# Kernel optimization log

Measured on AMD Instinct MI355X. Metric: run time of the kernel, lower is better.

Reference implementation:

```python
import jax, jax.numpy as jnp
import numpy as np

N = 20000


def _gcn_conv(x, edge_index, W, b):
    # add self loops
    n = x.shape[0]
    loops = jnp.arange(n, dtype=edge_index.dtype)
    row = jnp.concatenate([edge_index[0], loops])
    col = jnp.concatenate([edge_index[1], loops])
    # linear
    x = x @ W + b  # [N, C_out]
    # symmetric degree norm: deg computed over col (targets)
    deg = jax.ops.segment_sum(jnp.ones_like(col, dtype=x.dtype), col, num_segments=n)
    dinv = jnp.where(deg > 0, deg ** -0.5, 0.0)
    norm = dinv[row] * dinv[col]  # [E+N]
    # gather-scale-scatter (aggr='add' into col)
    msgs = norm[:, None] * x[row]  # [E+N, C_out]
    return jax.ops.segment_sum(msgs, col, num_segments=n)


def setup_inputs() -> dict:
    key = jax.random.key(0)
    k1, k2, k3, k4, k5, k6 = jax.random.split(key, 6)
    in_c, out_c = 256, 128
    hid = 2 * out_c
    x = jax.random.normal(k1, (N, in_c), dtype=jnp.float32)
    edge_index = jax.random.randint(k2, (2, 640000), 0, N, dtype=jnp.int64)
    s1 = 1.0 / np.sqrt(in_c)
    s2 = 1.0 / np.sqrt(hid)
    W1 = jax.random.uniform(k3, (in_c, hid), jnp.float32, -s1, s1)
    b1 = jax.random.uniform(k4, (hid,), jnp.float32, -s1, s1)
    W2 = jax.random.uniform(k5, (hid, out_c), jnp.float32, -s2, s2)
    b2 = jax.random.uniform(k6, (out_c,), jnp.float32, -s2, s2)
    return {"x": x, "edge_index": edge_index, "W1": W1, "b1": b1, "W2": W2, "b2": b2}


def reference(x, edge_index, W1, b1, W2, b2):
    h = jax.nn.relu(_gcn_conv(x, edge_index, W1, b1))
    return _gcn_conv(h, edge_index, W2, b2)
```

## Files before the change

### kernel.cpp

```cpp
#include <hip/hip_runtime.h>

#define CDIV(a,b) (((a)+(b)-1)/(b))

typedef _Float16 half4v __attribute__((ext_vector_type(4)));
typedef _Float16 half2v __attribute__((ext_vector_type(2)));
typedef _Float16 f16x8  __attribute__((ext_vector_type(8)));
typedef unsigned short ushort8v __attribute__((ext_vector_type(8)));
typedef float f32x4 __attribute__((ext_vector_type(4)));

__global__ void zero_kernel(int* __restrict__ p, int n) {
    int i = blockIdx.x * blockDim.x + threadIdx.x;
    if (i < n) p[i] = 0;
}

__global__ void hist_kernel(const int* __restrict__ coli, int* __restrict__ counts, int E) {
    int e = blockIdx.x * blockDim.x + threadIdx.x;
    if (e < E) atomicAdd(&counts[coli[e]], 1);
}

__global__ __launch_bounds__(1024) void scan_part(const int* __restrict__ counts,
                                                  int* __restrict__ offsets,
                                                  int* __restrict__ bsum,
                                                  float* __restrict__ dinv, int n) {
    __shared__ int wsum[16];
    int b = blockIdx.x, tid = threadIdx.x;
    int i = b * 1024 + tid;
    int lane = tid & 63, wid = tid >> 6;
    int v = (i < n) ? counts[i] : 0;
    if (i < n) dinv[i] = 1.0f / sqrtf((float)(v + 1));
    int x = v;
    #pragma unroll
    for (int off = 1; off < 64; off <<= 1) {
        int t = __shfl_up(x, off);
        if (lane >= off) x += t;
    }
    if (lane == 63) wsum[wid] = x;
    __syncthreads();
    if (tid == 0) {
        int run = 0;
        #pragma unroll
        for (int w = 0; w < 16; ++w) { int t = wsum[w]; wsum[w] = run; run += t; }
        bsum[b] = run;
    }
    __syncthreads();
    int incl = wsum[wid] + x;
    if (i < n) offsets[i + 1] = incl;
}

__global__ __launch_bounds__(1024) void scan_fix(const int* __restrict__ counts,
                                                 int* __restrict__ offsets,
                                                 const int* __restrict__ bsum,
                                                 int* __restrict__ nexta, int n) {
    int b = blockIdx.x, tid = threadIdx.x;
    int i = b * 1024 + tid;
    int pre = 0;
    for (int j = 0; j < b; ++j) pre += bsum[j];
    if (i == 0) offsets[0] = 0;
    if (i < n) {
        int incl = offsets[i + 1] + pre;
        offsets[i + 1] = incl;
        nexta[i] = incl - counts[i];
    }
}

__global__ void scatter_kernel(const int* __restrict__ rowi, const int* __restrict__ coli,
                               int* __restrict__ nexta, int* __restrict__ srcs, int E) {
    int e = blockIdx.x * blockDim.x + threadIdx.x;
    if (e < E) {
        int c = coli[e];
        int pos = atomicAdd(&nexta[c], 1);
        srcs[pos] = rowi[e];
    }
}

__global__ void tohalf_kernel(const float* __restrict__ in, _Float16* __restrict__ out, int n4) {
    int i = blockIdx.x * blockDim.x + threadIdx.x;
    if (i < n4) {
        float4 v = ((const float4*)in)[i];
        half4v h;
        h.x = (_Float16)v.x; h.y = (_Float16)v.y;
        h.z = (_Float16)v.z; h.w = (_Float16)v.w;
        ((half4v*)out)[i] = h;
    }
}

__global__ void wt_kernel(const float* __restrict__ W, _Float16* __restrict__ WT, int K, int N) {
    int idx = blockIdx.x * blockDim.x + threadIdx.x;
    if (idx < K * N) {
        int nrow = idx / K, k = idx - nrow * K;
        WT[idx] = (_Float16)W[(size_t)k * N + nrow];
    }
}

__global__ void agg1_f16(const _Float16* __restrict__ xh, const int* __restrict__ srcs,
                         const int* __restrict__ offsets, const float* __restrict__ dinv,
                         _Float16* __restrict__ xout, float* __restrict__ sarr,
                         int vpr, int n) {
    int gw   = blockIdx.x * (blockDim.x >> 6) + (threadIdx.x >> 6);
    int lane = threadIdx.x & 63;
    if (gw >= n) return;
    int c   = __builtin_amdgcn_readfirstlane(gw);
    int beg = __builtin_amdgcn_readfirstlane(offsets[c]);
    int end = __builtin_amdgcn_readfirstlane(offsets[c + 1]);
    const half4v* x4 = (const half4v*)xh;
    float4 acc = make_float4(0.f, 0.f, 0.f, 0.f);
    float wsum = 0.f;
    int i = beg;
    for (; i + 3 < end; i += 4) {
        int r0 = __builtin_amdgcn_readfirstlane(srcs[i + 0]);
        int r1 = __builtin_amdgcn_readfirstlane(srcs[i + 1]);
        int r2 = __builtin_amdgcn_readfirstlane(srcs[i + 2]);
        int r3 = __builtin_amdgcn_readfirstlane(srcs[i + 3]);
        float w0 = dinv[r0], w1 = dinv[r1], w2 = dinv[r2], w3 = dinv[r3];
        half4v v0 = x4[(size_t)r0 * vpr + lane];
        half4v v1 = x4[(size_t)r1 * vpr + lane];
        half4v v2 = x4[(size_t)r2 * vpr + lane];
        half4v v3 = x4[(size_t)r3 * vpr + lane];
        acc.x = fmaf(w0, (float)v0.x, acc.x); acc.y = fmaf(w0, (float)v0.y, acc.y);
        acc.z = fmaf(w0, (float)v0.z, acc.z); acc.w = fmaf(w0, (float)v0.w, acc.w);
        acc.x = fmaf(w1, (float)v1.x, acc.x); acc.y = fmaf(w1, (float)v1.y, acc.y);
        acc.z = fmaf(w1, (float)v1.z, acc.z); acc.w = fmaf(w1, (float)v1.w, acc.w);
        acc.x = fmaf(w2, (float)v2.x, acc.x); acc.y = fmaf(w2, (float)v2.y, acc.y);
        acc.z = fmaf(w2, (float)v2.z, acc.z); acc.w = fmaf(w2, (float)v2.w, acc.w);
        acc.x = fmaf(w3, (float)v3.x, acc.x); acc.y = fmaf(w3, (float)v3.y, acc.y);
        acc.z = fmaf(w3, (float)v3.z, acc.z); acc.w = fmaf(w3, (float)v3.w, acc.w);
        wsum += w0 + w1 + w2 + w3;
    }
    for (; i < end; ++i) {
        int r   = __builtin_amdgcn_readfirstlane(srcs[i]);
        float w = dinv[r];
        half4v v = x4[(size_t)r * vpr + lane];
        acc.x = fmaf(w, (float)v.x, acc.x); acc.y = fmaf(w, (float)v.y, acc.y);
        acc.z = fmaf(w, (float)v.z, acc.z); acc.w = fmaf(w, (float)v.w, acc.w);
        wsum += w;
    }
    float dc = dinv[c];
    half4v vc = x4[(size_t)c * vpr + lane];
    acc.x = fmaf(dc, (float)vc.x, acc.x); acc.y = fmaf(dc, (float)vc.y, acc.y);
    acc.z = fmaf(dc, (float)vc.z, acc.z); acc.w = fmaf(dc, (float)vc.w, acc.w);
    wsum += dc;
    half4v o;
    o.x = (_Float16)(acc.x * dc); o.y = (_Float16)(acc.y * dc);
    o.z = (_Float16)(acc.z * dc); o.w = (_Float16)(acc.w * dc);
    ((half4v*)xout)[(size_t)c * vpr + lane] = o;
    if (sarr && lane == 0) sarr[c] = dc * wsum;
}

__global__ void agg2_f16(const _Float16* __restrict__ zh, const int* __restrict__ srcs,
                         const int* __restrict__ offsets, const float* __restrict__ dinv,
                         float* __restrict__ xout, int vpr, int n) {
    int gw   = blockIdx.x * (blockDim.x >> 6) + (threadIdx.x >> 6);
    int lane = threadIdx.x & 63;
    if (gw >= n) return;
    int c   = __builtin_amdgcn_readfirstlane(gw);
    int beg = __builtin_amdgcn_readfirstlane(offsets[c]);
    int end = __builtin_amdgcn_readfirstlane(offsets[c + 1]);
    const half2v* x2 = (const half2v*)zh;
    float2 acc = make_float2(0.f, 0.f);
    int i = beg;
    for (; i + 3 < end; i += 4) {
        int r0 = __builtin_amdgcn_readfirstlane(srcs[i + 0]);
        int r1 = __builtin_amdgcn_readfirstlane(srcs[i + 1]);
        int r2 = __builtin_amdgcn_readfirstlane(srcs[i + 2]);
        int r3 = __builtin_amdgcn_readfirstlane(srcs[i + 3]);
        float w0 = dinv[r0], w1 = dinv[r1], w2 = dinv[r2], w3 = dinv[r3];
        half2v v0 = x2[(size_t)r0 * vpr + lane];
        half2v v1 = x2[(size_t)r1 * vpr + lane];
        half2v v2 = x2[(size_t)r2 * vpr + lane];
        half2v v3 = x2[(size_t)r3 * vpr + lane];
        acc.x = fmaf(w0, (float)v0.x, acc.x); acc.y = fmaf(w0, (float)v0.y, acc.y);
        acc.x = fmaf(w1, (float)v1.x, acc.x); acc.y = fmaf(w1, (float)v1.y, acc.y);
        acc.x = fmaf(w2, (float)v2.x, acc.x); acc.y = fmaf(w2, (float)v2.y, acc.y);
        acc.x = fmaf(w3, (float)v3.x, acc.x); acc.y = fmaf(w3, (float)v3.y, acc.y);
    }
    for (; i < end; ++i) {
        int r   = __builtin_amdgcn_readfirstlane(srcs[i]);
        float w = dinv[r];
        half2v v = x2[(size_t)r * vpr + lane];
        acc.x = fmaf(w, (float)v.x, acc.x); acc.y = fmaf(w, (float)v.y, acc.y);
    }
    float dc = dinv[c];
    half2v vc = x2[(size_t)c * vpr + lane];
    acc.x = fmaf(dc, (float)vc.x, acc.x); acc.y = fmaf(dc, (float)vc.y, acc.y);
    acc.x *= dc; acc.y *= dc;
    ((float2*)xout)[(size_t)c * vpr + lane] = acc;
}

template<int BM, int BN, bool RELU, bool SBIAS>
__global__ __launch_bounds__(256) void gemm_mfma(
        const _Float16* __restrict__ A, const _Float16* __restrict__ BT,
        const float* __restrict__ bias, const float* __restrict__ sarr,
        _Float16* __restrict__ C, int M, int K, int N) {
    constexpr int FM = BM / 2 / 16, FN = BN / 2 / 16;
    constexpr int APT = BM * 4 / 256, BPT = BN * 4 / 256;
    static_assert(BM % 32 == 0 && BN % 32 == 0, "wave tile divisibility");
    static_assert(BM * 4 % 256 == 0 && BN * 4 % 256 == 0, "staging divisibility");
    __shared__ unsigned short A_lds[BM * 40];
    __shared__ unsigned short B_lds[BN * 40];
    int tid  = threadIdx.x;
    int wid  = tid >> 6, lane = tid & 63;
    int wm   = wid >> 1, wn = wid & 1;
    int q    = lane >> 4, r = lane & 15;
    int m0   = blockIdx.x * BM, n0 = blockIdx.y * BN;

    f32x4 acc[FM][FN];
    #pragma unroll
    for (int i = 0; i < FM; ++i)
        #pragma unroll
        for (int j = 0; j < FN; ++j)
            acc[i][j] = (f32x4){0.f, 0.f, 0.f, 0.f};

    ushort8v areg[APT], breg[BPT];
    auto loadA = [&](int k0) {
        #pragma unroll
        for (int i = 0; i < APT; ++i) {
            int g = tid + i * 256;
            int row = g >> 2, slot = g & 3;
            int gm = m0 + row;
            if (gm < M) areg[i] = *(const ushort8v*)(A + (size_t)gm * K + k0 + slot * 8);
            else        areg[i] = (ushort8v){0,0,0,0,0,0,0,0};
        }
    };
    auto loadB = [&](int k0) {
        #pragma unroll
        for (int i = 0; i < BPT; ++i) {
            int g = tid + i * 256;
            int row = g >> 2, slot = g & 3;
            breg[i] = *(const ushort8v*)(BT + (size_t)(n0 + row) * K + k0 + slot * 8);
        }
    };

    loadA(0); loadB(0);
    int steps = K / 32;
    for (int s = 0; s < steps; ++s) {
        __syncthreads();
        #pragma unroll
        for (int i = 0; i < APT; ++i) {
            int g = tid + i * 256;
            *(ushort8v*)&A_lds[(g >> 2) * 40 + (g & 3) * 8] = areg[i];
        }
        #pragma unroll
        for (int i = 0; i < BPT; ++i) {
            int g = tid + i * 256;
            *(ushort8v*)&B_lds[(g >> 2) * 40 + (g & 3) * 8] = breg[i];
        }
        __syncthreads();
        if (s + 1 < steps) { loadA((s + 1) * 32); loadB((s + 1) * 32); }
        f16x8 af[FM], bf[FN];
        #pragma unroll
        for (int i = 0; i < FM; ++i)
            af[i] = *(const f16x8*)&A_lds[(wm * (BM / 2) + i * 16 + r) * 40 + q * 8];
        #pragma unroll
        for (int j = 0; j < FN; ++j)
            bf[j] = *(const f16x8*)&B_lds[(wn * (BN / 2) + j * 16 + r) * 40 + q * 8];
        #pragma unroll
        for (int i = 0; i < FM; ++i)
            #pragma unroll
            for (int j = 0; j < FN; ++j)
                acc[i][j] = __builtin_amdgcn_mfma_f32_16x16x32_f16(af[i], bf[j], acc[i][j], 0, 0, 0);
    }

    #pragma unroll
    for (int i = 0; i < FM; ++i) {
        int row_base = m0 + wm * (BM / 2) + i * 16 + q * 4;
        #pragma unroll
        for (int g = 0; g < 4; ++g) {
            int row = row_base + g;
            if (row >= M) continue;
            float sv = SBIAS ? sarr[row] : 1.f;
            #pragma unroll
            for (int j = 0; j < FN; ++j) {
                int col = n0 + wn * (BN / 2) + j * 16 + r;
                float v = acc[i][j][g] + sv * bias[col];
                if (RELU) v = fmaxf(v, 0.f);
                C[(size_t)row * N + col] = (_Float16)v;
            }
        }
    }
}

extern "C" void kernel_launch(void* const* d_in, const int* in_sizes, int n_in,
                              void* d_out, int out_size, void* d_ws, size_t ws_size,
                              hipStream_t stream) {
    const float* x  = (const float*)d_in[0];
    const int*   ei = (const int*)d_in[1];
    const float* W1 = (const float*)d_in[2];
    const float* b1 = (const float*)d_in[3];
    const float* W2 = (const float*)d_in[4];
    const float* b2 = (const float*)d_in[5];

    const int hid  = in_sizes[3];
    const int outc = in_sizes[5];
    const int inc  = in_sizes[2] / hid;
    const int n    = in_sizes[0] / inc;
    const int E    = in_sizes[1] / 2;
    const int* rowi = ei;
    const int* coli = ei + E;

    char* p = (char*)d_ws;
    auto carve = [&](size_t bytes) {
        char* q = p;
        p += (bytes + 255) & ~(size_t)255;
        return (void*)q;
    };
    int*      counts  = (int*)     carve((size_t)n * 4);
    int*      offsets = (int*)     carve((size_t)(n + 1) * 4);
    int*      nexta   = (int*)     carve((size_t)n * 4);
    int*      srcs    = (int*)     carve((size_t)E * 4);
    float*    dinv    = (float*)   carve((size_t)n * 4);
    float*    sarr    = (float*)   carve((size_t)n * 4);
    int*      bsum    = (int*)     carve((size_t)32 * 4);
    _Float16* xh      = (_Float16*)carve((size_t)n * inc * 2);
    _Float16* aggxh   = (_Float16*)carve((size_t)n * inc * 2);
    _Float16* hh      = (_Float16*)carve((size_t)n * hid * 2);
    _Float16* w1t     = (_Float16*)carve((size_t)inc * hid * 2);
    _Float16* w2t     = (_Float16*)carve((size_t)hid * outc * 2);
    _Float16* zh      = xh;

    const int SCAN_B = CDIV(n, 1024);

    zero_kernel<<<CDIV(n, 256), 256, 0, stream>>>(counts, n);
    hist_kernel<<<CDIV(E, 256), 256, 0, stream>>>(coli, counts, E);
    scan_part<<<SCAN_B, 1024, 0, stream>>>(counts, offsets, bsum, dinv, n);
    scan_fix<<<SCAN_B, 1024, 0, stream>>>(counts, offsets, bsum, nexta, n);
    scatter_kernel<<<CDIV(E, 256), 256, 0, stream>>>(rowi, coli, nexta, srcs, E);

    wt_kernel<<<CDIV(inc * hid, 256), 256, 0, stream>>>(W1, w1t, inc, hid);
    wt_kernel<<<CDIV(hid * outc, 256), 256, 0, stream>>>(W2, w2t, hid, outc);

    tohalf_kernel<<<CDIV(n * inc / 4, 256), 256, 0, stream>>>(x, xh, n * inc / 4);
    agg1_f16<<<CDIV(n, 4), 256, 0, stream>>>(xh, srcs, offsets, dinv, aggxh, sarr, inc / 4, n);
    dim3 g1(CDIV(n, 128), hid / 128);
    gemm_mfma<128, 128, true, true><<<g1, 256, 0, stream>>>(aggxh, w1t, b1, sarr, hh, n, inc, hid);

    dim3 g2(CDIV(n, 64), outc / 128);
    gemm_mfma<64, 128, false, false><<<g2, 256, 0, stream>>>(hh, w2t, b2, nullptr, zh, n, hid, outc);
    agg2_f16<<<CDIV(n, 4), 256, 0, stream>>>(zh, srcs, offsets, dinv, (float*)d_out, outc / 2, n);
}
```

Measured before the change: 236.2 us.

## Slice feature tables into channel chunks for cache-friendly gather aggregation

Stores the node features, both the half-precision input and the second GEMM output, in a channel-sliced layout of 8 slices of 32 or 16 channels. Each aggregation block now handles one slice, so each gathered table is small enough to stay resident in cache. Inside a wave, 8 edge groups each read 8 lanes, and the partial sums are combined with cross-lane shuffles. The prep kernels (fp16 conversion, weight transposes, zeroing) are merged into a single launch. The trade-offs are 8x more blocks, each re-reading the edge indices, plus shuffle reductions and a scattered store pattern in the second GEMM epilogue.

```diff
diff --git a/kernel.cpp b/kernel.cpp
--- a/kernel.cpp
+++ b/kernel.cpp
@@ -3,14 +3,40 @@
 #define CDIV(a,b) (((a)+(b)-1)/(b))
 
 typedef _Float16 half4v __attribute__((ext_vector_type(4)));
-typedef _Float16 half2v __attribute__((ext_vector_type(2)));
 typedef _Float16 f16x8  __attribute__((ext_vector_type(8)));
 typedef unsigned short ushort8v __attribute__((ext_vector_type(8)));
 typedef float f32x4 __attribute__((ext_vector_type(4)));
 
-__global__ void zero_kernel(int* __restrict__ p, int n) {
-    int i = blockIdx.x * blockDim.x + threadIdx.x;
-    if (i < n) p[i] = 0;
+__global__ void prep_kernel(const float* __restrict__ x, _Float16* __restrict__ xs,
+                            const float* __restrict__ W1, _Float16* __restrict__ w1t,
+                            const float* __restrict__ W2, _Float16* __restrict__ w2t,
+                            int* __restrict__ counts,
+                            int n, int inc, int hid, int outc) {
+    int idx = blockIdx.x * blockDim.x + threadIdx.x;
+    int n_xs = n * inc / 8;
+    int n_w1 = inc * hid;
+    int n_w2 = hid * outc;
+    if (idx < n_xs) {
+        int ipn  = inc / 8;
+        int node = idx / ipn;
+        int ch0  = (idx - node * ipn) * 8;
+        int s    = ch0 >> 5, wi = ch0 & 31;
+        const float4* xp = (const float4*)(x + (size_t)node * inc + ch0);
+        float4 a = xp[0], b = xp[1];
+        half4v h0, h1;
+        h0.x=(_Float16)a.x; h0.y=(_Float16)a.y; h0.z=(_Float16)a.z; h0.w=(_Float16)a.w;
+        h1.x=(_Float16)b.x; h1.y=(_Float16)b.y; h1.z=(_Float16)b.z; h1.w=(_Float16)b.w;
+        _Float16* dst = xs + ((size_t)s * n + node) * 32 + wi;
+        *(half4v*)dst = h0; *(half4v*)(dst + 4) = h1;
+    } else if ((idx -= n_xs) < n_w1) {
+        int nr = idx / inc, k = idx - nr * inc;
+        w1t[idx] = (_Float16)W1[(size_t)k * hid + nr];
+    } else if ((idx -= n_w1) < n_w2) {
+        int nr = idx / hid, k = idx - nr * hid;
+        w2t[idx] = (_Float16)W2[(size_t)k * outc + nr];
+    } else if ((idx -= n_w2) < n) {
+        counts[idx] = 0;
+    }
 }
 
 __global__ void hist_kernel(const int* __restrict__ coli, int* __restrict__ counts, int E) {
@@ -73,128 +99,72 @@
     }
 }
 
-__global__ void tohalf_kernel(const float* __restrict__ in, _Float16* __restrict__ out, int n4) {
-    int i = blockIdx.x * blockDim.x + threadIdx.x;
-    if (i < n4) {
-        float4 v = ((const float4*)in)[i];
-        half4v h;
-        h.x = (_Float16)v.x; h.y = (_Float16)v.y;
-        h.z = (_Float16)v.z; h.w = (_Float16)v.w;
-        ((half4v*)out)[i] = h;
-    }
-}
-
-__global__ void wt_kernel(const float* __restrict__ W, _Float16* __restrict__ WT, int K, int N) {
-    int idx = blockIdx.x * blockDim.x + threadIdx.x;
-    if (idx < K * N) {
-        int nrow = idx / K, k = idx - nrow * K;
-        WT[idx] = (_Float16)W[(size_t)k * N + nrow];
-    }
-}
-
-__global__ void agg1_f16(const _Float16* __restrict__ xh, const int* __restrict__ srcs,
-                         const int* __restrict__ offsets, const float* __restrict__ dinv,
-                         _Float16* __restrict__ xout, float* __restrict__ sarr,
-                         int vpr, int n) {
-    int gw   = blockIdx.x * (blockDim.x >> 6) + (threadIdx.x >> 6);
-    int lane = threadIdx.x & 63;
-    if (gw >= n) return;
-    int c   = __builtin_amdgcn_readfirstlane(gw);
-    int beg = __builtin_amdgcn_readfirstlane(offsets[c]);
-    int end = __builtin_amdgcn_readfirstlane(offsets[c + 1]);
-    const half4v* x4 = (const half4v*)xh;
-    float4 acc = make_float4(0.f, 0.f, 0.f, 0.f);
+template<int VEC, bool SARR, typename OUTT>
+__global__ __launch_bounds__(256) void agg_sliced(
+        const _Float16* __restrict__ xs, const int* __restrict__ srcs,
+        const int* __restrict__ offsets, const float* __restrict__ dinv,
+        OUTT* __restrict__ xout, float* __restrict__ sarr, int n) {
+    constexpr int RS = 8 * VEC;
+    constexpr int C  = 8 * RS;
+    typedef _Float16 hv __attribute__((ext_vector_type(VEC)));
+    typedef float    fv __attribute__((ext_vector_type(VEC)));
+    int wid  = threadIdx.x >> 6, lane = threadIdx.x & 63;
+    int s    = blockIdx.x & 7;
+    int c    = (blockIdx.x >> 3) * 4 + wid;
+    if (c >= n) return;
+    int g    = lane >> 3, t = lane & 7;
+    int beg  = __builtin_amdgcn_readfirstlane(offsets[c]);
+    int end  = __builtin_amdgcn_readfirstlane(offsets[c + 1]);
+    const _Float16* tab = xs + (size_t)s * n * RS;
+    float acc[VEC] = {};
     float wsum = 0.f;
-    int i = beg;
-    for (; i + 3 < end; i += 4) {
-        int r0 = __builtin_amdgcn_readfirstlane(srcs[i + 0]);
-        int r1 = __builtin_amdgcn_readfirstlane(srcs[i + 1]);
-        int r2 = __builtin_amdgcn_readfirstlane(srcs[i + 2]);
-        int r3 = __builtin_amdgcn_readfirstlane(srcs[i + 3]);
-        float w0 = dinv[r0], w1 = dinv[r1], w2 = dinv[r2], w3 = dinv[r3];
-        half4v v0 = x4[(size_t)r0 * vpr + lane];
-        half4v v1 = x4[(size_t)r1 * vpr + lane];
-        half4v v2 = x4[(size_t)r2 * vpr + lane];
-        half4v v3 = x4[(size_t)r3 * vpr + lane];
-        acc.x = fmaf(w0, (float)v0.x, acc.x); acc.y = fmaf(w0, (float)v0.y, acc.y);
-        acc.z = fmaf(w0, (float)v0.z, acc.z); acc.w = fmaf(w0, (float)v0.w, acc.w);
-        acc.x = fmaf(w1, (float)v1.x, acc.x); acc.y = fmaf(w1, (float)v1.y, acc.y);
-        acc.z = fmaf(w1, (float)v1.z, acc.z); acc.w = fmaf(w1, (float)v1.w, acc.w);
-        acc.x = fmaf(w2, (float)v2.x, acc.x); acc.y = fmaf(w2, (float)v2.y, acc.y);
-        acc.z = fmaf(w2, (float)v2.z, acc.z); acc.w = fmaf(w2, (float)v2.w, acc.w);
-        acc.x = fmaf(w3, (float)v3.x, acc.x); acc.y = fmaf(w3, (float)v3.y, acc.y);
-        acc.z = fmaf(w3, (float)v3.z, acc.z); acc.w = fmaf(w3, (float)v3.w, acc.w);
-        wsum += w0 + w1 + w2 + w3;
-    }
-    for (; i < end; ++i) {
-        int r   = __builtin_amdgcn_readfirstlane(srcs[i]);
-        float w = dinv[r];
-        half4v v = x4[(size_t)r * vpr + lane];
-        acc.x = fmaf(w, (float)v.x, acc.x); acc.y = fmaf(w, (float)v.y, acc.y);
-        acc.z = fmaf(w, (float)v.z, acc.z); acc.w = fmaf(w, (float)v.w, acc.w);
+    for (int i = beg; i < end; i += 8) {
+        int  e   = i + g;
+        bool val = e < end;
+        int  r   = val ? srcs[e] : c;
+        float w  = val ? dinv[r] : 0.f;
+        hv v = *(const hv*)(tab + (size_t)r * RS + t * VEC);
+        #pragma unroll
+        for (int k = 0; k < VEC; ++k) acc[k] = fmaf(w, (float)v[k], acc[k]);
         wsum += w;
     }
     float dc = dinv[c];
-    half4v vc = x4[(size_t)c * vpr + lane];
-    acc.x = fmaf(dc, (float)vc.x, acc.x); acc.y = fmaf(dc, (float)vc.y, acc.y);
-    acc.z = fmaf(dc, (float)vc.z, acc.z); acc.w = fmaf(dc, (float)vc.w, acc.w);
-    wsum += dc;
-    half4v o;
-    o.x = (_Float16)(acc.x * dc); o.y = (_Float16)(acc.y * dc);
-    o.z = (_Float16)(acc.z * dc); o.w = (_Float16)(acc.w * dc);
-    ((half4v*)xout)[(size_t)c * vpr + lane] = o;
-    if (sarr && lane == 0) sarr[c] = dc * wsum;
-}
-
-__global__ void agg2_f16(const _Float16* __restrict__ zh, const int* __restrict__ srcs,
-                         const int* __restrict__ offsets, const float* __restrict__ dinv,
-                         float* __restrict__ xout, int vpr, int n) {
-    int gw   = blockIdx.x * (blockDim.x >> 6) + (threadIdx.x >> 6);
-    int lane = threadIdx.x & 63;
-    if (gw >= n) return;
-    int c   = __builtin_amdgcn_readfirstlane(gw);
-    int beg = __builtin_amdgcn_readfirstlane(offsets[c]);
-    int end = __builtin_amdgcn_readfirstlane(offsets[c + 1]);
-    const half2v* x2 = (const half2v*)zh;
-    float2 acc = make_float2(0.f, 0.f);
-    int i = beg;
-    for (; i + 3 < end; i += 4) {
-        int r0 = __builtin_amdgcn_readfirstlane(srcs[i + 0]);
-        int r1 = __builtin_amdgcn_readfirstlane(srcs[i + 1]);
-        int r2 = __builtin_amdgcn_readfirstlane(srcs[i + 2]);
-        int r3 = __builtin_amdgcn_readfirstlane(srcs[i + 3]);
-        float w0 = dinv[r0], w1 = dinv[r1], w2 = dinv[r2], w3 = dinv[r3];
-        half2v v0 = x2[(size_t)r0 * vpr + lane];
-        half2v v1 = x2[(size_t)r1 * vpr + lane];
-        half2v v2 = x2[(size_t)r2 * vpr + lane];
-        half2v v3 = x2[(size_t)r3 * vpr + lane];
-        acc.x = fmaf(w0, (float)v0.x, acc.x); acc.y = fmaf(w0, (float)v0.y, acc.y);
-        acc.x = fmaf(w1, (float)v1.x, acc.x); acc.y = fmaf(w1, (float)v1.y, acc.y);
-        acc.x = fmaf(w2, (float)v2.x, acc.x); acc.y = fmaf(w2, (float)v2.y, acc.y);
-        acc.x = fmaf(w3, (float)v3.x, acc.x); acc.y = fmaf(w3, (float)v3.y, acc.y);
-    }
-    for (; i < end; ++i) {
-        int r   = __builtin_amdgcn_readfirstlane(srcs[i]);
-        float w = dinv[r];
-        half2v v = x2[(size_t)r * vpr + lane];
-        acc.x = fmaf(w, (float)v.x, acc.x); acc.y = fmaf(w, (float)v.y, acc.y);
-    }
-    float dc = dinv[c];
-    half2v vc = x2[(size_t)c * vpr + lane];
-    acc.x = fmaf(dc, (float)vc.x, acc.x); acc.y = fmaf(dc, (float)vc.y, acc.y);
-    acc.x *= dc; acc.y *= dc;
-    ((float2*)xout)[(size_t)c * vpr + lane] = acc;
-}
-
-template<int BM, int BN, bool RELU, bool SBIAS>
+    if (g == 0) {
+        hv vc = *(const hv*)(tab + (size_t)c * RS + t * VEC);
+        #pragma unroll
+        for (int k = 0; k < VEC; ++k) acc[k] = fmaf(dc, (float)vc[k], acc[k]);
+        wsum += dc;
+    }
+    #pragma unroll
+    for (int off = 8; off < 64; off <<= 1) {
+        #pragma unroll
+        for (int k = 0; k < VEC; ++k) acc[k] += __shfl_xor(acc[k], off);
+        wsum += __shfl_xor(wsum, off);
+    }
+    if (g == 0) {
+        if constexpr (sizeof(OUTT) == 2) {
+            hv o;
+            #pragma unroll
+            for (int k = 0; k < VEC; ++k) o[k] = (_Float16)(acc[k] * dc);
+            *(hv*)((_Float16*)xout + (size_t)c * C + s * RS + t * VEC) = o;
+        } else {
+            fv o;
+            #pragma unroll
+            for (int k = 0; k < VEC; ++k) o[k] = acc[k] * dc;
+            *(fv*)((float*)xout + (size_t)c * C + s * RS + t * VEC) = o;
+        }
+        if (SARR && s == 0 && lane == 0) sarr[c] = dc * wsum;
+    }
+}
+
+template<int BM, int BN, bool RELU, bool SBIAS, bool SLICED>
 __global__ __launch_bounds__(256) void gemm_mfma(
         const _Float16* __restrict__ A, const _Float16* __restrict__ BT,
         const float* __restrict__ bias, const float* __restrict__ sarr,
-        _Float16* __restrict__ C, int M, int K, int N) {
+        _Float16* __restrict__ C, int M, int K, int N, int tabn) {
     constexpr int FM = BM / 2 / 16, FN = BN / 2 / 16;
     constexpr int APT = BM * 4 / 256, BPT = BN * 4 / 256;
     static_assert(BM % 32 == 0 && BN % 32 == 0, "wave tile divisibility");
-    static_assert(BM * 4 % 256 == 0 && BN * 4 % 256 == 0, "staging divisibility");
     __shared__ unsigned short A_lds[BM * 40];
     __shared__ unsigned short B_lds[BN * 40];
     int tid  = threadIdx.x;
@@ -273,7 +243,9 @@
                 int col = n0 + wn * (BN / 2) + j * 16 + r;
                 float v = acc[i][j][g] + sv * bias[col];
                 if (RELU) v = fmaxf(v, 0.f);
-                C[(size_t)row * N + col] = (_Float16)v;
+                size_t addr = SLICED ? ((size_t)(col >> 4) * tabn + row) * 16 + (col & 15)
+                                     : (size_t)row * N + col;
+                C[addr] = (_Float16)v;
             }
         }
     }
@@ -306,34 +278,36 @@
     int*      counts  = (int*)     carve((size_t)n * 4);
     int*      offsets = (int*)     carve((size_t)(n + 1) * 4);
     int*      nexta   = (int*)     carve((size_t)n * 4);
-    int*      srcs    = (int*)     carve((size_t)E * 4);
+    int*      srcs    = (int*)     carve((size_t)(E + 8) * 4);
     float*    dinv    = (float*)   carve((size_t)n * 4);
     float*    sarr    = (float*)   carve((size_t)n * 4);
     int*      bsum    = (int*)     carve((size_t)32 * 4);
-    _Float16* xh      = (_Float16*)carve((size_t)n * inc * 2);
+    _Float16* xs      = (_Float16*)carve((size_t)n * inc * 2);
     _Float16* aggxh   = (_Float16*)carve((size_t)n * inc * 2);
     _Float16* hh      = (_Float16*)carve((size_t)n * hid * 2);
     _Float16* w1t     = (_Float16*)carve((size_t)inc * hid * 2);
     _Float16* w2t     = (_Float16*)carve((size_t)hid * outc * 2);
-    _Float16* zh      = xh;
+    _Float16* zs      = xs;
 
     const int SCAN_B = CDIV(n, 1024);
-
-    zero_kernel<<<CDIV(n, 256), 256, 0, stream>>>(counts, n);
+    const int PREP_T = n * inc / 8 + inc * hid + hid * outc + n;
+
+    prep_kernel<<<CDIV(PREP_T, 256), 256, 0, stream>>>(x, xs, W1, w1t, W2, w2t, counts,
+                                                       n, inc, hid, outc);
     hist_kernel<<<CDIV(E, 256), 256, 0, stream>>>(coli, counts, E);
     scan_part<<<SCAN_B, 1024, 0, stream>>>(counts, offsets, bsum, dinv, n);
     scan_fix<<<SCAN_B, 1024, 0, stream>>>(counts, offsets, bsum, nexta, n);
     scatter_kernel<<<CDIV(E, 256), 256, 0, stream>>>(rowi, coli, nexta, srcs, E);
 
-    wt_kernel<<<CDIV(inc * hid, 256), 256, 0, stream>>>(W1, w1t, inc, hid);
-    wt_kernel<<<CDIV(hid * outc, 256), 256, 0, stream>>>(W2, w2t, hid, outc);
-
-    tohalf_kernel<<<CDIV(n * inc / 4, 256), 256, 0, stream>>>(x, xh, n * inc / 4);
-    agg1_f16<<<CDIV(n, 4), 256, 0, stream>>>(xh, srcs, offsets, dinv, aggxh, sarr, inc / 4, n);
+    agg_sliced<4, true, _Float16><<<CDIV(n, 4) * 8, 256, 0, stream>>>(
+        xs, srcs, offsets, dinv, aggxh, sarr, n);
     dim3 g1(CDIV(n, 128), hid / 128);
-    gemm_mfma<128, 128, true, true><<<g1, 256, 0, stream>>>(aggxh, w1t, b1, sarr, hh, n, inc, hid);
+    gemm_mfma<128, 128, true, true, false><<<g1, 256, 0, stream>>>(
+        aggxh, w1t, b1, sarr, hh, n, inc, hid, 0);
 
     dim3 g2(CDIV(n, 64), outc / 128);
-    gemm_mfma<64, 128, false, false><<<g2, 256, 0, stream>>>(hh, w2t, b2, nullptr, zh, n, hid, outc);
-    agg2_f16<<<CDIV(n, 4), 256, 0, stream>>>(zh, srcs, offsets, dinv, (float*)d_out, outc / 2, n);
-}
+    gemm_mfma<64, 128, false, false, true><<<g2, 256, 0, stream>>>(
+        hh, w2t, b2, nullptr, zs, n, hid, outc, n);
+    agg_sliced<2, false, float><<<CDIV(n, 4) * 8, 256, 0, stream>>>(
+        zs, srcs, offsets, dinv, (float*)d_out, nullptr, n);
+}
```

After: 309.1 us. 30.8% more time.
